# Optimization experiments

Hardware: AMD Instinct MI355X
Metric: run time of the kernel (lower is better)

## Reference

```python
import jax, jax.numpy as jnp
import numpy as np

I, H, NH, A = 128, 2048, 2, 4   # input_size, hidden_size, n_hidden, alpha_dim
K = 2 * A * A                   # per-position theta entries
B = 8192


def make_masks():
    # MADE sequential-ordering masks, identical to DART.create_masks
    inp = np.arange(I)
    degrees = [inp] + [np.arange(H) % (I - 1) for _ in range(NH + 1)] + [np.arange(I) - 1]
    masks = [(d1[:, None] >= d0[None, :]).astype(np.float32)
             for d0, d1 in zip(degrees[:-1], degrees[1:])]
    # last mask repeated per theta entry: repeat(1, K).view(-1, H) == row-repeat
    masks[-1] = np.repeat(masks[-1], K, axis=0)
    return [jnp.asarray(m) for m in masks]


def setup_inputs() -> dict:
    key = jax.random.key(0)
    ks = jax.random.split(key, 5)
    x = jax.random.normal(ks[0], (B, I), dtype=jnp.float32)

    def lin(k, out_dim, in_dim):
        kw, kb = jax.random.split(k)
        s = 1.0 / np.sqrt(in_dim)
        W = jax.random.uniform(kw, (out_dim, in_dim), minval=-s, maxval=s, dtype=jnp.float32)
        b = jax.random.uniform(kb, (out_dim,), minval=-s, maxval=s, dtype=jnp.float32)
        return W, b

    W0, b0 = lin(ks[1], H, I)
    W1, b1 = lin(ks[2], H, H)
    W2, b2 = lin(ks[3], H, H)
    W3, b3 = lin(ks[4], I * K, H)
    return dict(x=x, W0=W0, b0=b0, W1=W1, b1=b1, W2=W2, b2=b2, W3=W3, b3=b3)


def logexpmm(a, b):
    # log-domain matmul: out[..., i, j] = logsumexp_k(a[..., i, k] + b[..., k, j])
    return jax.nn.logsumexp(a[..., :, :, None] + b[..., None, :, :], axis=-2)


def reference(x, W0, b0, W1, b1, W2, b2, W3, b3):
    m = make_masks()
    h = jax.nn.relu(x @ (m[0] * W0).T + b0)
    h = jax.nn.relu(h @ (m[1] * W1).T + b1)
    h = jax.nn.relu(h @ (m[2] * W2).T + b2)
    theta = (h @ (m[3] * W3).T + b3).reshape(-1, I, 2, A, A)
    mu, alpha = theta[:, :, 0], theta[:, :, 1]  # (B, I, A, A)

    LOG2PI = float(np.log(2.0 * np.pi))
    xe = x[:, :, None, None]
    # Normal(mu, exp(alpha)).log_prob(x) - log(alpha_dim)
    logp = (-0.5 * ((xe - mu) * jnp.exp(-alpha)) ** 2
            - alpha - 0.5 * LOG2PI - jnp.log(jnp.float32(A)))

    first = logp[:, 0, 0:1]        # (B, 1, A)
    last = logp[:, -1, :, 0:1]     # (B, A, 1)
    inner = jnp.swapaxes(logp[:, 1:-1], 0, 1)  # (I-2, B, A, A)

    def step(carry, mtx):
        return logexpmm(carry, mtx), None

    prod, _ = jax.lax.scan(step, inner[0], inner[1:])
    return logexpmm(first, logexpmm(prod, last))  # (B, 1, 1)
```

## Files before the change

### kernel.cpp

```cpp
#include <hip/hip_runtime.h>
#include <hip/hip_bf16.h>
#include <cstdint>
#include <cstddef>

#define AS1 __attribute__((address_space(1)))
#define AS3 __attribute__((address_space(3)))

typedef __bf16 bf16x8  __attribute__((ext_vector_type(8)));
typedef float  floatx4 __attribute__((ext_vector_type(4)));

__device__ __forceinline__ void load_lds16(const void* g, void* l) {
    __builtin_amdgcn_global_load_lds((AS1 void*)g, (AS3 void*)l, 16, 0, 0);
}

__device__ __forceinline__ float fexp2(float x) { return __builtin_amdgcn_exp2f(x); }
__device__ __forceinline__ float flog2(float x) { return __builtin_amdgcn_logf(x); }

#define LOG2E 1.4426950408889634f
#define LN2   0.6931471805599453f
#define C0K   2.3052328943245633f

__device__ __forceinline__ float logp2(float xv, float mu, float al) {
    float e = fexp2(-al * LOG2E);
    float z = (xv - mu) * e;
    return (-0.5f * z * z - al - C0K) * LOG2E;
}
__device__ __forceinline__ float lse4(float a0, float a1, float a2, float a3) {
    float mx = fmaxf(fmaxf(a0, a1), fmaxf(a2, a3));
    return mx + flog2(fexp2(a0 - mx) + fexp2(a1 - mx) +
                      fexp2(a2 - mx) + fexp2(a3 - mx));
}
__device__ __forceinline__ void lmm4(const float* Aa, const float* Bb, float* D) {
#pragma unroll
    for (int r = 0; r < 4; ++r)
#pragma unroll
        for (int c = 0; c < 4; ++c)
            D[r * 4 + c] = lse4(Aa[r * 4 + 0] + Bb[0 * 4 + c],
                                Aa[r * 4 + 1] + Bb[1 * 4 + c],
                                Aa[r * 4 + 2] + Bb[2 * 4 + c],
                                Aa[r * 4 + 3] + Bb[3 * 4 + c]);
}

__device__ __forceinline__ int resp_s(int p) {
    return p < 272 ? p / 17 : 16 + ((p - 272) >> 4);
}
__device__ __forceinline__ int invp_s(int p) {
    if (p < 272) { int d = p / 17; int r = p - d * 17;
                   return r < 16 ? d + r * 127 : 2032 + d; }
    int d = 16 + ((p - 272) >> 4); int j = (p - 272) & 15;
    return d + j * 127;
}
__device__ __forceinline__ int cnt_le(int D) {
    return D < 16 ? (D + 1) * 17 : 272 + ((D - 15) << 4);
}

__global__ __launch_bounds__(256)
void prep_all(const float* __restrict__ x,  const float* __restrict__ W0,
              const float* __restrict__ W1, const float* __restrict__ W2,
              const float* __restrict__ W3,
              __bf16* __restrict__ xb,  __bf16* __restrict__ w0m,
              __bf16* __restrict__ w1m, __bf16* __restrict__ w2m,
              __bf16* __restrict__ w3m)
{
    __shared__ float lds[2048];
    const int blk = blockIdx.x;
    const int tid = threadIdx.x;
    const int t8  = tid * 8;

    if (blk < 640) {
        bf16x8 o;
        if (blk < 512) {
            size_t base = (size_t)blk * 2048 + t8;
            floatx4 a = *(const floatx4*)(x + base);
            floatx4 b = *(const floatx4*)(x + base + 4);
#pragma unroll
            for (int j = 0; j < 4; ++j) { o[j] = (__bf16)a[j]; o[4 + j] = (__bf16)b[j]; }
            *(bf16x8*)(xb + base) = o;
        } else {
            long idx = (long)(blk - 512) * 2048 + t8;
            int p_n = (int)(idx >> 7);
            int c   = (int)(idx & 127);
            int dg  = resp_s(p_n);
            const float* s = W0 + (long)invp_s(p_n) * 128 + c;
            floatx4 a = *(const floatx4*)s;
            floatx4 b = *(const floatx4*)(s + 4);
#pragma unroll
            for (int j = 0; j < 8; ++j) {
                float v = j < 4 ? a[j] : b[j - 4];
                o[j] = (__bf16)((dg >= c + j) ? v : 0.0f);
            }
            *(bf16x8*)(w0m + idx) = o;
        }
        return;
    }

    const float* srow; __bf16* drow; int deg_n; bool strict;
    if (blk < 2688) {
        int p_n = blk - 640;
        srow = W1 + (size_t)invp_s(p_n) * 2048; drow = w1m + (size_t)p_n * 2048;
        deg_n = resp_s(p_n); strict = false;
    } else if (blk < 4736) {
        int p_n = blk - 2688;
        srow = W2 + (size_t)invp_s(p_n) * 2048; drow = w2m + (size_t)p_n * 2048;
        deg_n = resp_s(p_n); strict = false;
    } else {
        int n = blk - 4736;
        srow = W3 + (size_t)n * 2048; drow = w3m + (size_t)n * 2048;
        deg_n = n >> 5; strict = true;
    }
    floatx4 a = *(const floatx4*)(srow + t8);
    floatx4 b = *(const floatx4*)(srow + t8 + 4);
    *(floatx4*)&lds[t8]     = a;
    *(floatx4*)&lds[t8 + 4] = b;
    __syncthreads();
    bf16x8 o;
#pragma unroll
    for (int j = 0; j < 8; ++j) {
        int p = t8 + j;
        float v = lds[invp_s(p)];
        int dg = resp_s(p);
        bool keep = strict ? (deg_n > dg) : (deg_n >= dg);
        o[j] = (__bf16)(keep ? v : 0.0f);
    }
    *(bf16x8*)(drow + t8) = o;
}

template <bool RELU, bool OBF16, bool TLAYOUT, bool PERMBIAS, int LMODE>
__global__ __launch_bounds__(256, 4)
void gemm_bt(const __bf16* __restrict__ A, const __bf16* __restrict__ Bw,
             const float* __restrict__ bias, void* __restrict__ Cout,
             int N, int K)
{
    __shared__ __align__(16) __bf16 lsA[128 * 64];
    __shared__ __align__(16) __bf16 lsB[128 * 64];
    const int tid  = threadIdx.x;
    const int wave = tid >> 6;
    const int lane = tid & 63;
    const int bm = blockIdx.x;
    const int bn = (gridDim.y - 1) - blockIdx.y;
    const int wm = wave >> 1, wn = wave & 1;

    const int r8 = lane >> 3;
    const int cb = (lane & 7) ^ r8;
    const __bf16* gsrc[8];
    __bf16* ldst[8];
#pragma unroll
    for (int t = 0; t < 8; ++t) {
        int j = wave * 8 + t;
        if (j < 16) {
            int row = bm * 128 + j * 8 + r8;
            gsrc[t] = A + (size_t)row * K + cb * 8;
            ldst[t] = lsA + j * 512;
        } else {
            int jj = j - 16;
            int row = bn * 128 + jj * 8 + r8;
            gsrc[t] = Bw + (size_t)row * K + cb * 8;
            ldst[t] = lsB + jj * 512;
        }
    }

    const int fr  = lane & 15;
    const int ks  = lane >> 4;
    const int sx  = fr & 7;
    const int sl0 = ((ks)     ^ sx) * 8;
    const int sl1 = ((4 + ks) ^ sx) * 8;
    const __bf16* arow[4];
    const __bf16* brow[4];
#pragma unroll
    for (int i = 0; i < 4; ++i) {
        arow[i] = lsA + (wm * 64 + i * 16 + fr) * 64;
        brow[i] = lsB + (wn * 64 + i * 16 + fr) * 64;
    }

    floatx4 acc[4][4];
    const floatx4 vzero = {0.f, 0.f, 0.f, 0.f};
#pragma unroll
    for (int mi = 0; mi < 4; ++mi)
#pragma unroll
        for (int ni = 0; ni < 4; ++ni) acc[mi][ni] = vzero;

    const int nk = K >> 6;
    int limit;
    if (LMODE == 0)      limit = (cnt_le(resp_s(bn * 128 + 127)) + 63) >> 6;
    else if (LMODE == 1) { int D = 4 * bn + 2; if (D > 126) D = 126;
                           limit = (cnt_le(D) + 63) >> 6; }
    else                 limit = (resp_s(bn * 128 + 127) + 64) >> 6;
    if (limit > nk) limit = nk;

    for (int it = 0; it < limit; ++it) {
        const int kt = it << 6;
        __syncthreads();
#pragma unroll
        for (int t = 0; t < 8; ++t)
            load_lds16((const void*)(gsrc[t] + kt), (void*)ldst[t]);
        __syncthreads();
        bf16x8 af[4], bf[4];
#pragma unroll
        for (int i = 0; i < 4; ++i) af[i] = *(const bf16x8*)(arow[i] + sl0);
#pragma unroll
        for (int i = 0; i < 4; ++i) bf[i] = *(const bf16x8*)(brow[i] + sl0);
#pragma unroll
        for (int mi = 0; mi < 4; ++mi)
#pragma unroll
            for (int ni = 0; ni < 4; ++ni)
                acc[mi][ni] = __builtin_amdgcn_mfma_f32_16x16x32_bf16(
                    af[mi], bf[ni], acc[mi][ni], 0, 0, 0);
#pragma unroll
        for (int i = 0; i < 4; ++i) af[i] = *(const bf16x8*)(arow[i] + sl1);
#pragma unroll
        for (int i = 0; i < 4; ++i) bf[i] = *(const bf16x8*)(brow[i] + sl1);
#pragma unroll
        for (int mi = 0; mi < 4; ++mi)
#pragma unroll
            for (int ni = 0; ni < 4; ++ni)
                acc[mi][ni] = __builtin_amdgcn_mfma_f32_16x16x32_bf16(
                    af[mi], bf[ni], acc[mi][ni], 0, 0, 0);
    }

    const int cn  = lane & 15;
    const int cr4 = (lane >> 4) * 4;
#pragma unroll
    for (int ni = 0; ni < 4; ++ni) {
        int col = bn * 128 + wn * 64 + ni * 16 + cn;
        float bv = bias[PERMBIAS ? invp_s(col) : col];
#pragma unroll
        for (int mi = 0; mi < 4; ++mi) {
            int row0 = bm * 128 + wm * 64 + mi * 16 + cr4;
#pragma unroll
            for (int q = 0; q < 4; ++q) {
                float v = acc[mi][ni][q] + bv;
                if (RELU) v = fmaxf(v, 0.f);
                if (TLAYOUT) {
                    size_t addr = (size_t)(bm * 2 + wm) * ((size_t)N * 64)
                                + (size_t)col * 64 + (mi * 16 + cr4 + q);
                    ((__bf16*)Cout)[addr] = (__bf16)v;
                } else if (OBF16) {
                    ((__bf16*)Cout)[(size_t)(row0 + q) * N + col] = (__bf16)v;
                } else {
                    ((float*)Cout)[(size_t)(row0 + q) * N + col] = v;
                }
            }
        }
    }
}

__global__ __launch_bounds__(448)
void chain_all(const __bf16* __restrict__ th2,
               const float* __restrict__ x,
               float* __restrict__ out)
{
    __shared__ float xs[32 * 129];
    __shared__ float Pl[32 * 238];
    const int tid = threadIdx.x;
    const int blk = blockIdx.x;

    for (int idx = tid; idx < 4096; idx += 448) {
        int bl = idx >> 7, i = idx & 127;
        xs[bl * 129 + i] = x[(size_t)blk * 4096 + idx];
    }
    __syncthreads();

    const int s  = tid >> 5;
    const int bl = tid & 31;
    const int b64 = (blk & 1) * 32 + bl;
    const __bf16* tb = th2 + (size_t)(blk >> 1) * (4096 * 64) + b64;

    {
        const int i0 = 1 + s * 9;
        const __bf16* tp = tb + (size_t)i0 * 32 * 64;
        float M[4][4];
#pragma unroll
        for (int r = 0; r < 4; ++r)
#pragma unroll
            for (int c = 0; c < 4; ++c) M[r][c] = (r == c) ? 0.f : -1e30f;

        for (int ii = 0; ii < 9; ++ii) {
            float mu[16], al[16];
#pragma unroll
            for (int j = 0; j < 16; ++j) mu[j] = (float)tp[(size_t)j * 64];
#pragma unroll
            for (int j = 0; j < 16; ++j) al[j] = (float)tp[(size_t)(16 + j) * 64];
            float xv = xs[bl * 129 + i0 + ii];
            tp += 2048;
            float lp[16];
#pragma unroll
            for (int j = 0; j < 16; ++j) lp[j] = logp2(xv, mu[j], al[j]);
            float Mn[4][4];
#pragma unroll
            for (int r = 0; r < 4; ++r)
#pragma unroll
                for (int c = 0; c < 4; ++c)
                    Mn[r][c] = lse4(M[r][0] + lp[0 + c], M[r][1] + lp[4 + c],
                                    M[r][2] + lp[8 + c], M[r][3] + lp[12 + c]);
#pragma unroll
            for (int r = 0; r < 4; ++r)
#pragma unroll
                for (int c = 0; c < 4; ++c) M[r][c] = Mn[r][c];
        }
        float* pb = Pl + bl * 238 + s * 17;
#pragma unroll
        for (int r = 0; r < 4; ++r)
#pragma unroll
            for (int c = 0; c < 4; ++c) pb[r * 4 + c] = M[r][c];
    }
    __syncthreads();

    float Q[16];
    if (tid < 224) {
        const float* base = Pl + bl * 238;
        lmm4(base + (2 * s) * 17, base + (2 * s + 1) * 17, Q);
    }
    __syncthreads();
    if (tid < 224) {
        float* dst = Pl + bl * 238 + s * 17;
#pragma unroll
        for (int e = 0; e < 16; ++e) dst[e] = Q[e];
    }
    __syncthreads();

    if (tid < 32) {
        const float* base = Pl + tid * 238;
        float M[16], T[16];
#pragma unroll
        for (int e = 0; e < 16; ++e) M[e] = base[e];
#pragma unroll
        for (int j = 1; j < 7; ++j) {
            lmm4(M, base + j * 17, T);
#pragma unroll
            for (int e = 0; e < 16; ++e) M[e] = T[e];
        }
        const int bb64 = (blk & 1) * 32 + tid;
        const __bf16* tbb = th2 + (size_t)(blk >> 1) * (4096 * 64) + bb64;
        float x0 = xs[tid * 129 + 0];
        float xl = xs[tid * 129 + 127];
        float last[4], t4[4], f4[4];
#pragma unroll
        for (int c = 0; c < 4; ++c)
            last[c] = logp2(xl, (float)tbb[(size_t)(4064 + c * 4) * 64],
                                (float)tbb[(size_t)(4064 + 16 + c * 4) * 64]);
#pragma unroll
        for (int r = 0; r < 4; ++r)
            t4[r] = lse4(M[r * 4 + 0] + last[0], M[r * 4 + 1] + last[1],
                         M[r * 4 + 2] + last[2], M[r * 4 + 3] + last[3]);
#pragma unroll
        for (int r = 0; r < 4; ++r)
            f4[r] = logp2(x0, (float)tbb[(size_t)r * 64],
                              (float)tbb[(size_t)(16 + r) * 64]);
        out[blk * 32 + tid] = LN2 * lse4(f4[0] + t4[0], f4[1] + t4[1],
                                         f4[2] + t4[2], f4[3] + t4[3]);
    }
}

extern "C" void kernel_launch(void* const* d_in, const int* in_sizes, int n_in,
                              void* d_out, int out_size, void* d_ws, size_t ws_size,
                              hipStream_t stream)
{
    (void)in_sizes; (void)n_in; (void)out_size; (void)ws_size;
    const float* x  = (const float*)d_in[0];
    const float* W0 = (const float*)d_in[1];
    const float* b0 = (const float*)d_in[2];
    const float* W1 = (const float*)d_in[3];
    const float* b1 = (const float*)d_in[4];
    const float* W2 = (const float*)d_in[5];
    const float* b2 = (const float*)d_in[6];
    const float* W3 = (const float*)d_in[7];
    const float* b3 = (const float*)d_in[8];

    char* ws = (char*)d_ws;
    const size_t MB = 1024 * 1024;
    __bf16* h2  = (__bf16*)(ws + 0);
    __bf16* xb  = (__bf16*)(ws + 32 * MB);
    __bf16* w0m = (__bf16*)(ws + 34 * MB);
    __bf16* w1m = (__bf16*)(ws + 35 * MB);
    __bf16* w2m = (__bf16*)(ws + 43 * MB);
    __bf16* th  = (__bf16*)(ws + 0);
    __bf16* w3m = (__bf16*)(ws + 64 * MB);
    __bf16* h1  = (__bf16*)(ws + 80 * MB);
    __bf16* h3  = h1;

    prep_all<<<8832, 256, 0, stream>>>(x, W0, W1, W2, W3, xb, w0m, w1m, w2m, w3m);

    gemm_bt<true, true, false, true, 2><<<dim3(64, 16), 256, 0, stream>>>(
        xb, w0m, b0, h1, 2048, 128);
    gemm_bt<true, true, false, true, 0><<<dim3(64, 16), 256, 0, stream>>>(
        h1, w1m, b1, h2, 2048, 2048);
    gemm_bt<true, true, false, true, 0><<<dim3(64, 16), 256, 0, stream>>>(
        h2, w2m, b2, h3, 2048, 2048);
    gemm_bt<false, false, true, false, 1><<<dim3(64, 32), 256, 0, stream>>>(
        h3, w3m, b3, th, 4096, 2048);

    chain_all<<<256, 448, 0, stream>>>(th, x, (float*)d_out);
}
```

Baseline: 333.5 us.

## Add 256x128-tile 8-wave GEMM with ping-pong staged LDS pipeline for hidden layers

New measurement: 322.0 us. -3.4%, faster.

```diff
diff --git a/kernel.cpp b/kernel.cpp
--- a/kernel.cpp
+++ b/kernel.cpp
@@ -244,6 +244,178 @@
     }
 }
 
+#define CFENCE() asm volatile("" ::: "memory")
+#define BARX()  do { CFENCE(); __builtin_amdgcn_s_barrier(); CFENCE(); } while (0)
+#define WVM2()  asm volatile("s_waitcnt vmcnt(2)" ::: "memory")
+#define WVM0()  asm volatile("s_waitcnt vmcnt(0)" ::: "memory")
+#define WLGK()  asm volatile("s_waitcnt lgkmcnt(0)" ::: "memory")
+
+template <bool RELU, bool OBF16, bool TLAYOUT, bool PERMBIAS, int LMODE>
+__global__ __launch_bounds__(512)
+void gemm8p(const __bf16* __restrict__ A, const __bf16* __restrict__ Bw,
+            const float* __restrict__ bias, void* __restrict__ Cout,
+            int N, int K)
+{
+    __shared__ __align__(16) __bf16 ls[2 * 24576];
+    const int tid  = threadIdx.x;
+    const int wave = tid >> 6;
+    const int lane = tid & 63;
+    const int bm = blockIdx.x;
+    const int bn = (gridDim.y - 1) - blockIdx.y;
+    const int wm = wave >> 1, wn = wave & 1;
+
+    const int l8 = lane >> 3;
+    const int cb = (lane & 7) ^ l8;
+    const __bf16* gA[2][2];  int dA[2][2];
+    const __bf16* gB[2];     int dB[2];
+#pragma unroll
+    for (int h = 0; h < 2; ++h)
+#pragma unroll
+        for (int s = 0; s < 2; ++s) {
+            int rt = h * 128 + wave * 16 + s * 8;
+            gA[h][s] = A + (size_t)(bm * 256 + rt + l8) * K + cb * 8;
+            dA[h][s] = rt * 64;
+        }
+#pragma unroll
+    for (int s = 0; s < 2; ++s) {
+        int rt = wave * 16 + s * 8;
+        gB[s] = Bw + (size_t)(bn * 128 + rt + l8) * K + cb * 8;
+        dB[s] = 16384 + rt * 64;
+    }
+
+#define STG_A(buf, kt) do { \
+    load_lds16((const void*)(gA[0][0] + (kt)), (void*)(ls + (buf)*24576 + dA[0][0])); \
+    load_lds16((const void*)(gA[0][1] + (kt)), (void*)(ls + (buf)*24576 + dA[0][1])); \
+    load_lds16((const void*)(gA[1][0] + (kt)), (void*)(ls + (buf)*24576 + dA[1][0])); \
+    load_lds16((const void*)(gA[1][1] + (kt)), (void*)(ls + (buf)*24576 + dA[1][1])); } while (0)
+#define STG_B(buf, kt) do { \
+    load_lds16((const void*)(gB[0] + (kt)), (void*)(ls + (buf)*24576 + dB[0])); \
+    load_lds16((const void*)(gB[1] + (kt)), (void*)(ls + (buf)*24576 + dB[1])); } while (0)
+
+    const int fr  = lane & 15;
+    const int ks  = lane >> 4;
+    const int sx  = fr & 7;
+    const int sl0 = ((ks)     ^ sx) * 8;
+    const int sl1 = ((4 + ks) ^ sx) * 8;
+    int aoff[4], boff[4];
+#pragma unroll
+    for (int i = 0; i < 4; ++i) {
+        aoff[i] = (wm * 64 + i * 16 + fr) * 64;
+        boff[i] = 16384 + (wn * 64 + i * 16 + fr) * 64;
+    }
+
+    floatx4 acc[4][4];
+    const floatx4 vzero = {0.f, 0.f, 0.f, 0.f};
+#pragma unroll
+    for (int mi = 0; mi < 4; ++mi)
+#pragma unroll
+        for (int ni = 0; ni < 4; ++ni) acc[mi][ni] = vzero;
+
+    bf16x8 bfr[4][2], afr[2][2];
+
+#define DSRD_B(buf) do { \
+    _Pragma("unroll") \
+    for (int ni = 0; ni < 4; ++ni) { \
+        bfr[ni][0] = *(const bf16x8*)(ls + (buf)*24576 + boff[ni] + sl0); \
+        bfr[ni][1] = *(const bf16x8*)(ls + (buf)*24576 + boff[ni] + sl1); } } while (0)
+#define DSRD_A(buf, q) do { \
+    _Pragma("unroll") \
+    for (int j = 0; j < 2; ++j) { \
+        afr[j][0] = *(const bf16x8*)(ls + (buf)*24576 + aoff[2*(q)+j] + sl0); \
+        afr[j][1] = *(const bf16x8*)(ls + (buf)*24576 + aoff[2*(q)+j] + sl1); } } while (0)
+#define MFMA16(q) do { \
+    __builtin_amdgcn_s_setprio(1); \
+    _Pragma("unroll") \
+    for (int j = 0; j < 2; ++j) \
+    _Pragma("unroll") \
+    for (int ni = 0; ni < 4; ++ni) { \
+        acc[2*(q)+j][ni] = __builtin_amdgcn_mfma_f32_16x16x32_bf16( \
+            afr[j][0], bfr[ni][0], acc[2*(q)+j][ni], 0, 0, 0); \
+        acc[2*(q)+j][ni] = __builtin_amdgcn_mfma_f32_16x16x32_bf16( \
+            afr[j][1], bfr[ni][1], acc[2*(q)+j][ni], 0, 0, 0); } \
+    __builtin_amdgcn_s_setprio(0); } while (0)
+
+    const int nk = K >> 6;
+    int limit;
+    if (LMODE == 0)      limit = (cnt_le(resp_s(bn * 128 + 127)) + 63) >> 6;
+    else if (LMODE == 1) { int D = 4 * bn + 2; if (D > 126) D = 126;
+                           limit = (cnt_le(D) + 63) >> 6; }
+    else                 limit = (resp_s(bn * 128 + 127) + 64) >> 6;
+    if (limit > nk) limit = nk;
+    const int NT = limit;
+
+    STG_B(0, 0);
+    STG_A(0, 0);
+    if (NT > 1) { STG_B(1, 64); WVM2(); } else { WVM0(); }
+    BARX();
+
+    for (int t = 0; ; t += 2) {
+        const int kt1 = (t + 1) << 6, kt2 = (t + 2) << 6, kt3 = (t + 3) << 6;
+        const bool has1 = t + 1 < NT, has2 = t + 2 < NT, has3 = t + 3 < NT;
+
+        DSRD_B(0);
+        DSRD_A(0, 0);
+        if (has1) STG_A(1, kt1);
+        BARX(); WLGK();
+        MFMA16(0);
+        BARX();
+
+        DSRD_A(0, 1);
+        if (has2) STG_B(0, kt2);
+        BARX(); WLGK();
+        MFMA16(1);
+        if (!has1) break;
+        if (has2) WVM2(); else WVM0();
+        BARX();
+
+        DSRD_B(1);
+        DSRD_A(1, 0);
+        if (has2) STG_A(0, kt2);
+        BARX(); WLGK();
+        MFMA16(0);
+        BARX();
+
+        DSRD_A(1, 1);
+        if (has3) STG_B(1, kt3);
+        BARX(); WLGK();
+        MFMA16(1);
+        if (!has2) break;
+        if (has3) WVM2(); else WVM0();
+        BARX();
+    }
+
+    const int cn  = lane & 15;
+    const int cr4 = (lane >> 4) * 4;
+#pragma unroll
+    for (int ni = 0; ni < 4; ++ni) {
+        int col = bn * 128 + wn * 64 + ni * 16 + cn;
+        float bv = bias[PERMBIAS ? invp_s(col) : col];
+#pragma unroll
+        for (int mi = 0; mi < 4; ++mi) {
+            int row0 = bm * 256 + wm * 64 + mi * 16 + cr4;
+#pragma unroll
+            for (int q = 0; q < 4; ++q) {
+                float v = acc[mi][ni][q] + bv;
+                if (RELU) v = fmaxf(v, 0.f);
+                if (TLAYOUT) {
+                    size_t addr = (size_t)(bm * 4 + wm) * ((size_t)N * 64)
+                                + (size_t)col * 64 + (mi * 16 + cr4 + q);
+                    ((__bf16*)Cout)[addr] = (__bf16)v;
+                } else if (OBF16) {
+                    ((__bf16*)Cout)[(size_t)(row0 + q) * N + col] = (__bf16)v;
+                } else {
+                    ((float*)Cout)[(size_t)(row0 + q) * N + col] = v;
+                }
+            }
+        }
+    }
+#undef STG_A
+#undef STG_B
+#undef DSRD_B
+#undef DSRD_A
+#undef MFMA16
+}
+
 __global__ __launch_bounds__(448)
 void chain_all(const __bf16* __restrict__ th2,
                const float* __restrict__ x,
@@ -382,11 +554,11 @@
 
     gemm_bt<true, true, false, true, 2><<<dim3(64, 16), 256, 0, stream>>>(
         xb, w0m, b0, h1, 2048, 128);
-    gemm_bt<true, true, false, true, 0><<<dim3(64, 16), 256, 0, stream>>>(
+    gemm8p<true, true, false, true, 0><<<dim3(32, 16), 512, 0, stream>>>(
         h1, w1m, b1, h2, 2048, 2048);
-    gemm_bt<true, true, false, true, 0><<<dim3(64, 16), 256, 0, stream>>>(
+    gemm8p<true, true, false, true, 0><<<dim3(32, 16), 512, 0, stream>>>(
         h2, w2m, b2, h3, 2048, 2048);
-    gemm_bt<false, false, true, false, 1><<<dim3(64, 32), 256, 0, stream>>>(
+    gemm8p<false, false, true, false, 1><<<dim3(32, 32), 512, 0, stream>>>(
         h3, w3m, b3, th, 4096, 2048);
 
     chain_all<<<256, 448, 0, stream>>>(th, x, (float*)d_out);
```
